# Kernel tuning notes

Measured on AMD Instinct MI355X. Metric: run time of the kernel, lower is better.

Reference implementation:

```python
import jax, jax.numpy as jnp
import numpy as np

B, N, H, D, F = 32, 128, 256, 256, 512   # batch, nodes, gru hidden, latent dim, mlp hidden
SUP = 0.5                                 # ancestor_suppression_strength
EPS = 1e-6


def _gru(x, h, Wx, Wh, bx, bh):
    """torch.nn.GRUCell math; x,h: [..., H]."""
    gx = x @ Wx + bx
    gh = h @ Wh + bh
    rx, ux, nx = jnp.split(gx, 3, axis=-1)
    rh, uh, nh = jnp.split(gh, 3, axis=-1)
    r = jax.nn.sigmoid(rx + rh)
    u = jax.nn.sigmoid(ux + uh)
    n = jnp.tanh(nx + r * nh)
    return (1.0 - u) * n + u * h


def setup_inputs() -> dict:
    key = jax.random.key(0)
    ks = jax.random.split(key, 12)
    rn = lambda k, shape, fan: jax.random.normal(k, shape, jnp.float32) * (fan ** -0.5)
    return {
        "z": jax.random.normal(ks[0], (B, D), jnp.float32),
        "targets": jax.random.randint(ks[1], (B, N, N), 0, 2, jnp.int32),
        "W_init": rn(ks[2], (D, H), D),
        "b_init": jnp.zeros((H,), jnp.float32),
        "Wx": rn(ks[3], (H, 3 * H), H),
        "Wh": rn(ks[4], (H, 3 * H), H),
        "bx": jnp.zeros((3 * H,), jnp.float32),
        "bh": jnp.zeros((3 * H,), jnp.float32),
        "W1": rn(ks[5], (2 * H + D, F), 2 * H + D),
        "b1": jnp.zeros((F,), jnp.float32),
        "W2": rn(ks[6], (F, 1), F),
        "b2": jnp.zeros((1,), jnp.float32),
    }


def reference(z, targets, W_init, b_init, Wx, Wh, bx, bh, W1, b1, W2, b2):
    # teacher-forcing link targets: strictly lower-triangular (parents have smaller index)
    tgt = jnp.tril(targets.astype(jnp.float32), k=-1)  # [B,N,N]
    idx = jnp.arange(N)

    def decode_one(z1, t1):  # z1:[D], t1:[N,N]
        h0 = jnp.tanh(z1 @ W_init + b_init)                      # decoder_init: z -> node-0 state
        states0 = jnp.zeros((N, H), jnp.float32).at[0].set(h0)
        A0 = jnp.zeros((N, N), jnp.float32)                      # ancestor bitset: A[i,j]=1 iff j ancestor of i

        def step(carry, t):
            states, A, ll = carry
            m = (idx < t).astype(jnp.float32)                    # existing-node mask
            pooled = (states * m[:, None]).sum(0) / m.sum()      # mean aggregation
            h_prov = _gru(pooled, h0, Wx, Wh, bx, bh)            # provisional new-node state
            # parent logits: MLP([h_new, h_j, z]) for every existing node j
            feat = jnp.concatenate([jnp.broadcast_to(h_prov, (N, H)), states,
                                    jnp.broadcast_to(z1, (N, D))], axis=-1)   # [N, 2H+D]
            logits = (jax.nn.relu(feat @ W1 + b1) @ W2 + b2)[:, 0]            # [N]
            row = t1[t]                                          # teacher-forced parents of node t
            anc = jnp.minimum(row @ A, 1.0)                      # j already ancestor of a chosen parent
            q = jnp.clip(jax.nn.sigmoid(logits) * (1.0 - SUP * anc), EPS, 1.0 - EPS)
            ll = ll + (m * (row * jnp.log(q) + (1.0 - row) * jnp.log1p(-q))).sum()
            A = A.at[t].set(jnp.minimum(row + row @ A, 1.0))     # ancestors(t) = parents U their ancestors
            states = states.at[t].set(h_prov)
            m2 = (idx <= t).astype(jnp.float32)[:, None]
            pooled2 = (states * m2).sum(0) / m2.sum()
            upd = _gru(jnp.broadcast_to(pooled2, (N, H)), states, Wx, Wh, bx, bh)
            states = m2 * upd + (1.0 - m2) * states              # propagate info among generated nodes
            return (states, A, ll), None

        (states, A, ll), _ = jax.lax.scan(step, (states0, A0, jnp.zeros((), jnp.float32)),
                                          jnp.arange(1, N))
        return t1, ll                                            # link matrix (teacher forced), log-likelihood

    L, ll = jax.vmap(decode_one)(z, tgt)
    return L, ll
```

## Files before the change

### kernel.cpp

```cpp
#include <hip/hip_runtime.h>
#include <hip/hip_bf16.h>
#include <math.h>

#define Bz 32
#define Nn 128
#define Hh 256
#define Dd 256
#define Ff 512
#define Gg 768
#define NT 512

typedef short v8s __attribute__((ext_vector_type(8)));
typedef float f4  __attribute__((ext_vector_type(4)));
#define MFMA(a,b,c) __builtin_amdgcn_mfma_f32_16x16x32_bf16(a,b,c,0,0,0)

#define WS_H0    0
#define WS_GH0   (WS_H0 + Bz*Hh)
#define WS_ZW1   (WS_GH0 + Bz*Gg)
#define WS_GXP   (WS_ZW1 + Bz*Ff)
#define WS_LOGP  (WS_GXP + Bz*8*Gg)
#define WS_BAR   (WS_LOGP + Bz*8*Nn)
#define WS_XS    (WS_BAR + Bz*32)
#define WS_WB    (WS_XS + Bz*16384)

#define SM_SW    0
#define SM_SST   81920
#define SM_NLDS  147456
#define SM_GXF   155648
#define SM_HPF   158720
#define SM_GX2   159232
#define SM_BASE  159616
#define SM_BHS   159872
#define SM_PSN   160256
#define SM_LOGI  160384
#define SM_RBIT  160896
#define SM_ANCW  160928
#define SM_AMASK 160960
#define SMEM_SZ  163008

__device__ __forceinline__ unsigned short f2bf(float x) {
  unsigned u = __float_as_uint(x);
  u = u + 0x7fffu + ((u >> 16) & 1u);
  return (unsigned short)(u >> 16);
}
__device__ __forceinline__ unsigned pack2(float e, float o) {
  return (unsigned)f2bf(e) | ((unsigned)f2bf(o) << 16);
}
__device__ __forceinline__ unsigned pkbf(float x, float y) {
  __hip_bfloat162 h = __float22bfloat162_rn(make_float2(x, y));
  union { __hip_bfloat162 h; unsigned u; } c; c.h = h; return c.u;
}
__device__ __forceinline__ float bf2f(unsigned short s) {
  return __uint_as_float(((unsigned)s) << 16);
}
__device__ __forceinline__ float sigm(float x) { return 1.0f / (1.0f + __expf(-x)); }
__device__ __forceinline__ float tanh_fast(float x) { return 2.0f / (1.0f + __expf(-2.0f*x)) - 1.0f; }
__device__ __forceinline__ v8s u4v(uint4 q) { union { uint4 q; v8s v; } c; c.q = q; return c.v; }

__device__ __forceinline__ void ast32(unsigned* p, unsigned v) {
  __hip_atomic_store(p, v, __ATOMIC_RELAXED, __HIP_MEMORY_SCOPE_AGENT);
}
__device__ __forceinline__ unsigned ald32(const unsigned* p) {
  return __hip_atomic_load(p, __ATOMIC_RELAXED, __HIP_MEMORY_SCOPE_AGENT);
}
__device__ __forceinline__ void ast64(unsigned long long* p, unsigned long long v) {
  __hip_atomic_store(p, v, __ATOMIC_RELAXED, __HIP_MEMORY_SCOPE_AGENT);
}
__device__ __forceinline__ unsigned long long ald64(const unsigned long long* p) {
  return __hip_atomic_load(p, __ATOMIC_RELAXED, __HIP_MEMORY_SCOPE_AGENT);
}

__device__ __forceinline__ void bbar(unsigned* cnt, unsigned& seq)
{
  __builtin_amdgcn_s_waitcnt(0x0F70);
  __syncthreads();
  seq += 8;
  if (threadIdx.x == 0) {
    __hip_atomic_fetch_add(cnt, 1u, __ATOMIC_RELAXED, __HIP_MEMORY_SCOPE_AGENT);
    while (__hip_atomic_load(cnt, __ATOMIC_RELAXED, __HIP_MEMORY_SCOPE_AGENT) < seq)
      __builtin_amdgcn_s_sleep(1);
  }
  __syncthreads();
}

__global__ void __launch_bounds__(256) prep_init(
    const int* __restrict__ tg, const float* __restrict__ Wx,
    const float* __restrict__ Wh, const float* __restrict__ W1,
    float* __restrict__ ws, float* __restrict__ out)
{
  const int stride = gridDim.x * blockDim.x;
  const int t0 = blockIdx.x * blockDim.x + threadIdx.x;

  for (int i = t0; i < Bz*Nn*Nn; i += stride) {
    int col = i & (Nn-1), row = (i >> 7) & (Nn-1);
    out[i] = (col < row) ? (float)tg[i] : 0.0f;
  }
  for (int i = t0; i < Bz; i += stride) out[Bz*Nn*Nn + i] = 0.0f;

  unsigned* BARu = (unsigned*)(ws + WS_BAR);
  for (int i = t0; i < Bz*32; i += stride) BARu[i] = 0u;

  unsigned* Wb = (unsigned*)(ws + WS_WB);
  for (int i = t0; i < 160*2048; i += stride) {
    int jw = i & 3, l = (i >> 2) & 63, ks = (i >> 8) & 7, nt = i >> 11;
    int k = ks*32 + (l >> 4)*8 + 2*jw;
    int n16 = l & 15;
    float lo, hi;
    if (nt < 48)       { int c = nt*16 + n16;        lo = Wh[k*Gg + c];      hi = Wh[(k+1)*Gg + c]; }
    else if (nt < 80)  { int f = (nt-48)*16 + n16;   lo = W1[(Hh+k)*Ff + f]; hi = W1[(Hh+k+1)*Ff + f]; }
    else if (nt < 128) { int c = (nt-80)*16 + n16;   lo = Wx[k*Gg + c];      hi = Wx[(k+1)*Gg + c]; }
    else               { int f = (nt-128)*16 + n16;  lo = W1[k*Ff + f];      hi = W1[(k+1)*Ff + f]; }
    Wb[i] = pack2(lo, hi);
  }
}

__global__ void __launch_bounds__(256) prep_batch(
    const float* __restrict__ z, const float* __restrict__ Wi,
    const float* __restrict__ bi, const float* __restrict__ Wh,
    const float* __restrict__ bh, const float* __restrict__ W1,
    float* __restrict__ ws)
{
  const int b = blockIdx.x, tid = threadIdx.x;
  __shared__ float zs[Dd], h0s[Hh];
  zs[tid] = z[b*Dd + tid];
  __syncthreads();
  float acc = bi[tid];
  for (int d = 0; d < Dd; ++d) acc = fmaf(zs[d], Wi[d*Hh + tid], acc);
  const float h0 = tanhf(acc);
  h0s[tid] = h0;
  ws[WS_H0 + b*Hh + tid] = h0;
  __syncthreads();
  for (int g = tid; g < Gg; g += 256) {
    float a = bh[g];
    for (int h = 0; h < Hh; ++h) a = fmaf(h0s[h], Wh[h*Gg + g], a);
    ws[WS_GH0 + b*Gg + g] = a;
  }
  for (int f = tid; f < Ff; f += 256) {
    float a = 0.0f;
    for (int d = 0; d < Dd; ++d) a = fmaf(zs[d], W1[(2*Hh + d)*Ff + f], a);
    ws[WS_ZW1 + b*Ff + f] = a;
  }
}

__global__ void __launch_bounds__(NT) decoder_main(
    const int* __restrict__ tg,
    const float* __restrict__ bx, const float* __restrict__ bh,
    const float* __restrict__ b1, const float* __restrict__ W2,
    const float* __restrict__ b2,
    float* __restrict__ ws, float* __restrict__ out)
{
  const int blk = blockIdx.x;
  const int b = blk & 31, r = blk >> 5;
  const int tid = threadIdx.x;
  const int lane = tid & 63, wv = tid >> 6;
  const int c16 = lane & 15, quad = lane >> 4;

  extern __shared__ char smem[];
  uint4* SW4 = (uint4*)(smem + SM_SW);
  unsigned short* SST = (unsigned short*)(smem + SM_SST);
  unsigned long long* SST64 = (unsigned long long*)(smem + SM_SST);
  unsigned short* NLDS = (unsigned short*)(smem + SM_NLDS);
  unsigned* NLDSu = (unsigned*)(smem + SM_NLDS);
  unsigned long long* NLDS64 = (unsigned long long*)(smem + SM_NLDS);
  float* GXF  = (float*)(smem + SM_GXF);
  unsigned short* HPF = (unsigned short*)(smem + SM_HPF);
  float* GX2  = (float*)(smem + SM_GX2);
  float* BASE = (float*)(smem + SM_BASE);
  float* BHS  = (float*)(smem + SM_BHS);
  float* PSN  = (float*)(smem + SM_PSN);
  float* LOGI = (float*)(smem + SM_LOGI);
  unsigned* RBIT  = (unsigned*)(smem + SM_RBIT);
  unsigned* ANCW  = (unsigned*)(smem + SM_ANCW);
  unsigned* AMASK = (unsigned*)(smem + SM_AMASK);

  const float* __restrict__ h0g  = ws + WS_H0  + b*Hh;
  const float* __restrict__ gh0g = ws + WS_GH0 + b*Gg;
  const float* __restrict__ zW1g = ws + WS_ZW1 + b*Ff;
  unsigned* GXPown = (unsigned*)(ws + WS_GXP) + b*8*Gg + r*Gg;
  const unsigned long long* GXP64 = (const unsigned long long*)((unsigned*)(ws + WS_GXP) + b*8*Gg);
  unsigned* LOGPg = (unsigned*)(ws + WS_LOGP) + b*8*Nn;
  unsigned long long* LOGP64 = (unsigned long long*)LOGPg;
  unsigned* bar = (unsigned*)(ws + WS_BAR) + b*32;
  unsigned long long* XS64 = (unsigned long long*)(ws + WS_XS) + b*8192;
  const uint4* WB4 = (const uint4*)(ws + WS_WB);

  for (int i = tid; i < 16384; i += NT) ((unsigned*)SST)[i] = 0u;
  for (int i = tid; i < 5120; i += NT) {
    const int lt = i >> 9, q = i & 511;
    int gt;
    if (lt < 6) { const int gate = lt >> 1, tt = lt & 1; gt = gate*16 + 2*r + tt; }
    else        { gt = 48 + 4*r + (lt - 6); }
    SW4[lt*512 + q] = WB4[gt*512 + q];
  }
  for (int i = tid; i < Nn*4; i += NT) AMASK[i] = 0u;
  if (tid < 96) BHS[tid] = bh[(tid >> 5)*256 + 32*r + (tid & 31)];
  float w2r[4];
  #pragma unroll
  for (int ft = 0; ft < 4; ++ft) w2r[ft] = W2[64*r + ft*16 + c16];
  const float b2v = b2[0];
  unsigned bseq = 0;
  __syncthreads();
  if (tid < Hh) {
    const int c = tid;
    SST[(c>>5)*512 + ((c>>3)&3)*128 + (c&7)] = f2bf(h0g[c]);
  }
  if (tid < 32) PSN[tid] = h0g[32*r + tid];
  __syncthreads();
  {
    union { unsigned u[4]; v8s v; } cv;
    const float4 a0 = *(const float4*)(PSN + quad*8);
    const float4 a1 = *(const float4*)(PSN + quad*8 + 4);
    cv.u[0] = pkbf(a0.x, a0.y); cv.u[1] = pkbf(a0.z, a0.w);
    cv.u[2] = pkbf(a1.x, a1.y); cv.u[3] = pkbf(a1.z, a1.w);
    const v8s avp = cv.v;
    #pragma unroll
    for (int k2 = 0; k2 < 6; ++k2) {
      const int nt = wv*6 + k2;
      f4 c = {0.0f,0.0f,0.0f,0.0f};
      c = MFMA(avp, u4v(WB4[(80 + nt)*512 + r*64 + lane]), c);
      if (quad == 0) ast32(GXPown + nt*16 + c16, __float_as_uint(c[0]));
    }
  }
  if (tid < 128) ast64(XS64 + r*128 + tid, SST64[r*128 + tid]);
  bbar(bar, bseq);

  for (int t = 1; t < Nn; ++t) {
    const int par = (t & 1) * 4;
    const float invt  = 1.0f / (float)t;
    const float invt1 = 1.0f / (float)(t + 1);
    const int Mtot = (t + 16) >> 4;
    const int Mlog = (t + 15) >> 4;
    const int mtc = Mtot - 1;

    for (int i = tid; i < Mlog*1024; i += NT) {
      if (((i >> 7) & 7) != r) SST64[i] = ald64(XS64 + i);
    }
    if (tid < 384) {
      float s0 = 0.0f, s1 = 0.0f;
      #pragma unroll
      for (int rr = 0; rr < 8; ++rr) {
        const unsigned long long v = ald64(GXP64 + rr*384 + tid);
        s0 += __uint_as_float((unsigned)v);
        s1 += __uint_as_float((unsigned)(v >> 32));
      }
      GXF[2*tid]   = s0;
      GXF[2*tid+1] = s1;
    } else {
      const int j = tid - 384;
      const int val = (j < t) ? tg[b*Nn*Nn + t*Nn + j] : 0;
      const unsigned long long bal = __ballot(val != 0);
      if (lane == 0) {
        RBIT[par + (wv - 6)*2]     = (unsigned)bal;
        RBIT[par + (wv - 6)*2 + 1] = (unsigned)(bal >> 32);
      }
      LOGI[j] = 0.0f;
      if (j < 32) PSN[j] = 0.0f;
      if (j < 4) ANCW[par + j] = 0u;
    }
    if (t > 1 && r == ((t - 1) & 7)) {
      const int pp = par ^ 4;
      float term = 0.0f;
      if (tid < (t - 1)) {
        float lsum = b2v;
        #pragma unroll
        for (int rr = 0; rr < 8; ++rr)
          lsum += __uint_as_float(ald32(LOGPg + rr*Nn + tid));
        const float anc = (float)((ANCW[pp + (tid >> 5)] >> (tid & 31)) & 1u);
        float q = sigm(lsum) * (1.0f - 0.5f*anc);
        q = fminf(fmaxf(q, 1e-6f), 1.0f - 1e-6f);
        const unsigned rb = (RBIT[pp + (tid >> 5)] >> (tid & 31)) & 1u;
        term = rb ? logf(q) : log1pf(-q);
      }
      if (wv < 2) {
        #pragma unroll
        for (int off = 32; off; off >>= 1) term += __shfl_down(term, off);
        if (lane == 0) atomicAdd(&out[Bz*Nn*Nn + b], term);
      }
    }
    __syncthreads();

    if (tid < 256) {
      const int hc = tid;
      const float rv = sigm(GXF[hc]*invt + bx[hc] + gh0g[hc]);
      const float uv = sigm(GXF[256+hc]*invt + bx[256+hc] + gh0g[256+hc]);
      const float nv = tanh_fast(GXF[512+hc]*invt + bx[512+hc] + rv*gh0g[512+hc]);
      HPF[hc] = f2bf((1.0f - uv)*nv + uv*h0g[hc]);
    } else if (tid < 384) {
      const int j = tid - 256;
      if (j < t && ((RBIT[par + (j >> 5)] >> (j & 31)) & 1u)) {
        atomicOr(&ANCW[par+0], AMASK[j*4+0]); atomicOr(&ANCW[par+1], AMASK[j*4+1]);
        atomicOr(&ANCW[par+2], AMASK[j*4+2]); atomicOr(&ANCW[par+3], AMASK[j*4+3]);
      }
    }
    __syncthreads();

    if (tid < 256) {
      const int c = tid;
      SST[(mtc*8 + (c>>5))*512 + (((c>>3)&3)*16 + (t&15))*8 + (c&7)] = HPF[c];
    } else {
      NLDSu[mtc*256 + (tid - 256)] = 0u;
    }
    if (wv < 2) {
      const unsigned rbv = (RBIT[par + (tid >> 5)] >> (tid & 31)) & 1u;
      const unsigned long long bal = __ballot(tid < t && rbv);
      if (lane == 0) {
        AMASK[t*4 + 2*wv]     = (unsigned)bal         | ANCW[par + 2*wv];
        AMASK[t*4 + 2*wv + 1] = (unsigned)(bal >> 32) | ANCW[par + 2*wv + 1];
      }
    }
    {
      v8s av[8];
      #pragma unroll
      for (int ks = 0; ks < 8; ++ks) av[ks] = *(const v8s*)(HPF + ks*32 + quad*8);
      for (int j = wv; j < 10; j += 8) {
        if (j < 6) {
          const int g = j >> 1, tt = j & 1;
          const uint4* Bp = WB4 + (80 + g*16 + 2*r + tt)*512 + lane;
          f4 c = {0.0f,0.0f,0.0f,0.0f};
          #pragma unroll
          for (int ks = 0; ks < 8; ++ks) c = MFMA(av[ks], u4v(Bp[ks*64]), c);
          if (quad == 0) {
            const int col = g*256 + 32*r + tt*16 + c16;
            GX2[g*32 + tt*16 + c16] = (c[0] + GXF[col])*invt1 + bx[col];
          }
        } else {
          const int ft = j - 6;
          const uint4* Bp = WB4 + (128 + 4*r + ft)*512 + lane;
          f4 c = {0.0f,0.0f,0.0f,0.0f};
          #pragma unroll
          for (int ks = 0; ks < 8; ++ks) c = MFMA(av[ks], u4v(Bp[ks*64]), c);
          if (quad == 0) {
            const int f = 64*r + ft*16 + c16;
            BASE[ft*16 + c16] = c[0] + zW1g[f] + b1[f];
          }
        }
      }
    }
    __syncthreads();

    const int nG = (Mtot + 1) >> 1;
    const int nL = (Mlog + 1) >> 1;
    const int njobs = nG + nL;
    for (int j = wv; j < njobs; j += 8) {
      if (j < nG) {
        const int mt0 = 2*j, mt1 = mt0 + 1;
        const bool do1 = (mt1 < Mtot);
        f4 acc[12];
        #pragma unroll
        for (int i = 0; i < 12; ++i) acc[i] = (f4){0.0f,0.0f,0.0f,0.0f};
        #pragma unroll
        for (int ks = 0; ks < 8; ++ks) {
          const v8s a0 = *(const v8s*)(SST + (mt0*8 + ks)*512 + lane*8);
          const v8s b0 = u4v(SW4[(0*8 + ks)*64 + lane]);
          const v8s b1v = u4v(SW4[(1*8 + ks)*64 + lane]);
          const v8s b2v2 = u4v(SW4[(2*8 + ks)*64 + lane]);
          const v8s b3 = u4v(SW4[(3*8 + ks)*64 + lane]);
          const v8s b4 = u4v(SW4[(4*8 + ks)*64 + lane]);
          const v8s b5 = u4v(SW4[(5*8 + ks)*64 + lane]);
          acc[0] = MFMA(a0, b0, acc[0]); acc[1] = MFMA(a0, b1v, acc[1]);
          acc[2] = MFMA(a0, b2v2, acc[2]); acc[3] = MFMA(a0, b3, acc[3]);
          acc[4] = MFMA(a0, b4, acc[4]); acc[5] = MFMA(a0, b5, acc[5]);
          if (do1) {
            const v8s a1 = *(const v8s*)(SST + (mt1*8 + ks)*512 + lane*8);
            acc[6]  = MFMA(a1, b0, acc[6]);  acc[7]  = MFMA(a1, b1v, acc[7]);
            acc[8]  = MFMA(a1, b2v2, acc[8]);  acc[9]  = MFMA(a1, b3, acc[9]);
            acc[10] = MFMA(a1, b4, acc[10]); acc[11] = MFMA(a1, b5, acc[11]);
          }
        }
        #pragma unroll
        for (int s = 0; s < 2; ++s) {
          if (s == 1 && !do1) break;
          const int mt = s ? mt1 : mt0;
          const f4* ac = acc + 6*s;
          #pragma unroll
          for (int ct = 0; ct < 2; ++ct) {
            const int hcl = ct*16 + c16;
            const f4 cr = ac[0 + ct], cu = ac[2 + ct], cn = ac[4 + ct];
            const float gxr = GX2[hcl], gxu = GX2[32+hcl], gxn = GX2[64+hcl];
            const float bhr = BHS[hcl], bhu = BHS[32+hcl], bhn = BHS[64+hcl];
            float colsum = 0.0f;
            #pragma unroll
            for (int rg = 0; rg < 4; ++rg) {
              const int row = mt*16 + quad*4 + rg;
              if (row <= t) {
                const int spi = ((hcl>>3)*16 + quad*4 + rg)*8 + (hcl & 7);
                const float old = bf2f(SST[(mt*8 + r)*512 + spi]);
                const float rv = sigm(gxr + cr[rg] + bhr);
                const float uv = sigm(gxu + cu[rg] + bhu);
                const float nv = tanh_fast(gxn + rv*(cn[rg] + bhn));
                const float ns = (1.0f-uv)*nv + uv*old;
                NLDS[mt*512 + spi] = f2bf(ns);
                colsum += ns;
              }
            }
            colsum += __shfl_down(colsum, 16);
            colsum += __shfl_down(colsum, 32);
            if (lane < 16) atomicAdd(&PSN[ct*16 + lane], colsum);
          }
        }
      } else {
        const int jj = j - nG;
        const int mt0 = 2*jj, mt1 = mt0 + 1;
        const bool do1 = (mt1 < Mlog);
        f4 acc[8];
        #pragma unroll
        for (int i = 0; i < 8; ++i) acc[i] = (f4){0.0f,0.0f,0.0f,0.0f};
        #pragma unroll
        for (int ks = 0; ks < 8; ++ks) {
          const v8s a0 = *(const v8s*)(SST + (mt0*8 + ks)*512 + lane*8);
          const v8s c0 = u4v(SW4[(6*8 + ks)*64 + lane]);
          const v8s c1 = u4v(SW4[(7*8 + ks)*64 + lane]);
          const v8s c2 = u4v(SW4[(8*8 + ks)*64 + lane]);
          const v8s c3 = u4v(SW4[(9*8 + ks)*64 + lane]);
          acc[0] = MFMA(a0, c0, acc[0]); acc[1] = MFMA(a0, c1, acc[1]);
          acc[2] = MFMA(a0, c2, acc[2]); acc[3] = MFMA(a0, c3, acc[3]);
          if (do1) {
            const v8s a1 = *(const v8s*)(SST + (mt1*8 + ks)*512 + lane*8);
            acc[4] = MFMA(a1, c0, acc[4]); acc[5] = MFMA(a1, c1, acc[5]);
            acc[6] = MFMA(a1, c2, acc[6]); acc[7] = MFMA(a1, c3, acc[7]);
          }
        }
        #pragma unroll
        for (int s = 0; s < 2; ++s) {
          if (s == 1 && !do1) break;
          const int mt = s ? mt1 : mt0;
          const f4* ac = acc + 4*s;
          #pragma unroll
          for (int rg = 0; rg < 4; ++rg) {
            float v = fmaxf(ac[0][rg] + BASE[c16],    0.0f)*w2r[0]
                    + fmaxf(ac[1][rg] + BASE[16+c16], 0.0f)*w2r[1]
                    + fmaxf(ac[2][rg] + BASE[32+c16], 0.0f)*w2r[2]
                    + fmaxf(ac[3][rg] + BASE[48+c16], 0.0f)*w2r[3];
            v += __shfl_xor(v, 1); v += __shfl_xor(v, 2);
            v += __shfl_xor(v, 4); v += __shfl_xor(v, 8);
            const int row = mt*16 + quad*4 + rg;
            if (c16 == 0 && row < t) atomicAdd(&LOGI[row], v);
          }
        }
      }
    }
    __syncthreads();

    {
      union { unsigned u[4]; v8s v; } cv;
      const float4 a0 = *(const float4*)(PSN + quad*8);
      const float4 a1 = *(const float4*)(PSN + quad*8 + 4);
      cv.u[0] = pkbf(a0.x, a0.y); cv.u[1] = pkbf(a0.z, a0.w);
      cv.u[2] = pkbf(a1.x, a1.y); cv.u[3] = pkbf(a1.z, a1.w);
      const v8s avp = cv.v;
      #pragma unroll
      for (int k2 = 0; k2 < 6; ++k2) {
        const int nt = wv*6 + k2;
        f4 c = {0.0f,0.0f,0.0f,0.0f};
        c = MFMA(avp, u4v(WB4[(80 + nt)*512 + r*64 + lane]), c);
        if (quad == 0) ast32(GXPown + nt*16 + c16, __float_as_uint(c[0]));
      }
    }
    for (int i = tid; i < Mtot*128; i += NT) {
      const int mt = i >> 7, q = i & 127;
      const unsigned long long v = NLDS64[i];
      ast64(XS64 + (mt*8 + r)*128 + q, v);
      SST64[(mt*8 + r)*128 + q] = v;
    }
    if (tid < 64) ast64(LOGP64 + r*64 + tid, ((const unsigned long long*)LOGI)[tid]);
    bbar(bar, bseq);
  }

  if (r == 7) {
    const int tl = Nn - 1;
    const int pp = (tl & 1) * 4;
    float term = 0.0f;
    if (tid < tl) {
      float lsum = b2v;
      #pragma unroll
      for (int rr = 0; rr < 8; ++rr)
        lsum += __uint_as_float(ald32(LOGPg + rr*Nn + tid));
      const float anc = (float)((ANCW[pp + (tid >> 5)] >> (tid & 31)) & 1u);
      float q = sigm(lsum) * (1.0f - 0.5f*anc);
      q = fminf(fmaxf(q, 1e-6f), 1.0f - 1e-6f);
      const unsigned rb = (RBIT[pp + (tid >> 5)] >> (tid & 31)) & 1u;
      term = rb ? logf(q) : log1pf(-q);
    }
    if (wv < 2) {
      #pragma unroll
      for (int off = 32; off; off >>= 1) term += __shfl_down(term, off);
      if (lane == 0) atomicAdd(&out[Bz*Nn*Nn + b], term);
    }
  }
}

extern "C" void kernel_launch(void* const* d_in, const int* in_sizes, int n_in,
                              void* d_out, int out_size, void* d_ws, size_t ws_size,
                              hipStream_t stream)
{
  const float* z  = (const float*)d_in[0];
  const int*   tg = (const int*)  d_in[1];
  const float* Wi = (const float*)d_in[2];
  const float* bi = (const float*)d_in[3];
  const float* Wx = (const float*)d_in[4];
  const float* Wh = (const float*)d_in[5];
  const float* bx = (const float*)d_in[6];
  const float* bh = (const float*)d_in[7];
  const float* W1 = (const float*)d_in[8];
  const float* b1 = (const float*)d_in[9];
  const float* W2 = (const float*)d_in[10];
  const float* b2 = (const float*)d_in[11];
  float* out = (float*)d_out;
  float* ws  = (float*)d_ws;

  hipFuncSetAttribute((const void*)decoder_main,
                      hipFuncAttributeMaxDynamicSharedMemorySize, SMEM_SZ);

  hipLaunchKernelGGL(prep_init, dim3(512), dim3(256), 0, stream, tg, Wx, Wh, W1, ws, out);
  hipLaunchKernelGGL(prep_batch, dim3(Bz), dim3(256), 0, stream, z, Wi, bi, Wh, bh, W1, ws);

  void* args[] = { (void*)&tg, (void*)&bx, (void*)&bh, (void*)&b1,
                   (void*)&W2, (void*)&b2, (void*)&ws, (void*)&out };
  hipLaunchCooperativeKernel((void*)decoder_main, dim3(256), dim3(NT),
                             args, SMEM_SZ, stream);
}
```

Before: 2.044 ms.

## Overlap new-node GRU with state-update MFMAs and drop a per-step barrier

Restructures each decode step so waves 0-5 start the existing-node GRU and logit MFMAs immediately after the first barrier. Meanwhile waves 6-7 compute the provisional node state, its own Wh projection (GHT) and the gx/zW1 projections. The new node's GRU update is split out and done separately by one wave. Ancestor-mask propagation moves into the target-loading wave via shuffle-OR, which removes the atomicOr phase and one __syncthreads. The GXP and LOGP exchange buffers are double-buffered by step parity so the log-likelihood reduction can move after the barrier-bracketed section, at the cost of more workspace, more registers and a more intricate job assignment.

```diff
diff --git a/kernel.cpp b/kernel.cpp
--- a/kernel.cpp
+++ b/kernel.cpp
@@ -18,8 +18,8 @@
 #define WS_GH0   (WS_H0 + Bz*Hh)
 #define WS_ZW1   (WS_GH0 + Bz*Gg)
 #define WS_GXP   (WS_ZW1 + Bz*Ff)
-#define WS_LOGP  (WS_GXP + Bz*8*Gg)
-#define WS_BAR   (WS_LOGP + Bz*8*Nn)
+#define WS_LOGP  (WS_GXP + Bz*2*8*Gg)
+#define WS_BAR   (WS_LOGP + Bz*2*8*Nn)
 #define WS_XS    (WS_BAR + Bz*32)
 #define WS_WB    (WS_XS + Bz*16384)
 
@@ -29,14 +29,15 @@
 #define SM_GXF   155648
 #define SM_HPF   158720
 #define SM_GX2   159232
-#define SM_BASE  159616
-#define SM_BHS   159872
-#define SM_PSN   160256
-#define SM_LOGI  160384
-#define SM_RBIT  160896
-#define SM_ANCW  160928
-#define SM_AMASK 160960
-#define SMEM_SZ  163008
+#define SM_GHT   159616
+#define SM_BASE  160000
+#define SM_BHS   160256
+#define SM_PSN   160640
+#define SM_LOGI  160768
+#define SM_RBIT  161280
+#define SM_ANCW  161312
+#define SM_AMASK 161376
+#define SMEM_SZ  163424
 
 __device__ __forceinline__ unsigned short f2bf(float x) {
   unsigned u = __float_as_uint(x);
@@ -142,6 +143,97 @@
   }
 }
 
+__device__ __forceinline__ void G_mfma(const unsigned short* SST, const uint4* SW4,
+    int mt0, bool do1, int lane, f4* acc)
+{
+  #pragma unroll
+  for (int ks = 0; ks < 8; ++ks) {
+    const v8s a0 = *(const v8s*)(SST + (mt0*8 + ks)*512 + lane*8);
+    const v8s w0 = u4v(SW4[(0*8 + ks)*64 + lane]);
+    const v8s w1 = u4v(SW4[(1*8 + ks)*64 + lane]);
+    const v8s w2 = u4v(SW4[(2*8 + ks)*64 + lane]);
+    const v8s w3 = u4v(SW4[(3*8 + ks)*64 + lane]);
+    const v8s w4 = u4v(SW4[(4*8 + ks)*64 + lane]);
+    const v8s w5 = u4v(SW4[(5*8 + ks)*64 + lane]);
+    acc[0] = MFMA(a0,w0,acc[0]); acc[1] = MFMA(a0,w1,acc[1]);
+    acc[2] = MFMA(a0,w2,acc[2]); acc[3] = MFMA(a0,w3,acc[3]);
+    acc[4] = MFMA(a0,w4,acc[4]); acc[5] = MFMA(a0,w5,acc[5]);
+    if (do1) {
+      const v8s a1 = *(const v8s*)(SST + ((mt0+1)*8 + ks)*512 + lane*8);
+      acc[6]  = MFMA(a1,w0,acc[6]);  acc[7]  = MFMA(a1,w1,acc[7]);
+      acc[8]  = MFMA(a1,w2,acc[8]);  acc[9]  = MFMA(a1,w3,acc[9]);
+      acc[10] = MFMA(a1,w4,acc[10]); acc[11] = MFMA(a1,w5,acc[11]);
+    }
+  }
+}
+
+__device__ __forceinline__ void G_epi(const f4* ac, int mt, int t, int r,
+    int quad, int c16, int lane, const float* GX2, const float* BHS,
+    const unsigned short* SST, unsigned short* NLDS, float* PSN)
+{
+  #pragma unroll
+  for (int ct = 0; ct < 2; ++ct) {
+    const int hcl = ct*16 + c16;
+    const f4 cr = ac[0 + ct], cu = ac[2 + ct], cn = ac[4 + ct];
+    const float gxr = GX2[hcl], gxu = GX2[32+hcl], gxn = GX2[64+hcl];
+    const float bhr = BHS[hcl], bhu = BHS[32+hcl], bhn = BHS[64+hcl];
+    float colsum = 0.0f;
+    #pragma unroll
+    for (int rg = 0; rg < 4; ++rg) {
+      const int row = mt*16 + quad*4 + rg;
+      if (row < t) {
+        const int spi = ((hcl>>3)*16 + quad*4 + rg)*8 + (hcl & 7);
+        const float old = bf2f(SST[(mt*8 + r)*512 + spi]);
+        const float rv = sigm(gxr + cr[rg] + bhr);
+        const float uv = sigm(gxu + cu[rg] + bhu);
+        const float nv = tanh_fast(gxn + rv*(cn[rg] + bhn));
+        const float ns = (1.0f-uv)*nv + uv*old;
+        NLDS[mt*512 + spi] = f2bf(ns);
+        colsum += ns;
+      }
+    }
+    colsum += __shfl_down(colsum, 16);
+    colsum += __shfl_down(colsum, 32);
+    if (lane < 16) atomicAdd(&PSN[ct*16 + lane], colsum);
+  }
+}
+
+__device__ __forceinline__ void L_mfma(const unsigned short* SST, const uint4* SW4,
+    int mt0, bool do1, int lane, f4* acc)
+{
+  #pragma unroll
+  for (int ks = 0; ks < 8; ++ks) {
+    const v8s a0 = *(const v8s*)(SST + (mt0*8 + ks)*512 + lane*8);
+    const v8s c0 = u4v(SW4[(6*8 + ks)*64 + lane]);
+    const v8s c1 = u4v(SW4[(7*8 + ks)*64 + lane]);
+    const v8s c2 = u4v(SW4[(8*8 + ks)*64 + lane]);
+    const v8s c3 = u4v(SW4[(9*8 + ks)*64 + lane]);
+    acc[0] = MFMA(a0,c0,acc[0]); acc[1] = MFMA(a0,c1,acc[1]);
+    acc[2] = MFMA(a0,c2,acc[2]); acc[3] = MFMA(a0,c3,acc[3]);
+    if (do1) {
+      const v8s a1 = *(const v8s*)(SST + ((mt0+1)*8 + ks)*512 + lane*8);
+      acc[4] = MFMA(a1,c0,acc[4]); acc[5] = MFMA(a1,c1,acc[5]);
+      acc[6] = MFMA(a1,c2,acc[6]); acc[7] = MFMA(a1,c3,acc[7]);
+    }
+  }
+}
+
+__device__ __forceinline__ void L_epi(const f4* ac, int mt, int t,
+    int quad, int c16, const float* BASE, const float* w2r, float* LOGI)
+{
+  #pragma unroll
+  for (int rg = 0; rg < 4; ++rg) {
+    float v = fmaxf(ac[0][rg] + BASE[c16],    0.0f)*w2r[0]
+            + fmaxf(ac[1][rg] + BASE[16+c16], 0.0f)*w2r[1]
+            + fmaxf(ac[2][rg] + BASE[32+c16], 0.0f)*w2r[2]
+            + fmaxf(ac[3][rg] + BASE[48+c16], 0.0f)*w2r[3];
+    v += __shfl_xor(v, 1); v += __shfl_xor(v, 2);
+    v += __shfl_xor(v, 4); v += __shfl_xor(v, 8);
+    const int row = mt*16 + quad*4 + rg;
+    if (c16 == 0 && row < t) atomicAdd(&LOGI[row], v);
+  }
+}
+
 __global__ void __launch_bounds__(NT) decoder_main(
     const int* __restrict__ tg,
     const float* __restrict__ bx, const float* __restrict__ bh,
@@ -165,6 +257,7 @@
   float* GXF  = (float*)(smem + SM_GXF);
   unsigned short* HPF = (unsigned short*)(smem + SM_HPF);
   float* GX2  = (float*)(smem + SM_GX2);
+  float* GHT  = (float*)(smem + SM_GHT);
   float* BASE = (float*)(smem + SM_BASE);
   float* BHS  = (float*)(smem + SM_BHS);
   float* PSN  = (float*)(smem + SM_PSN);
@@ -176,15 +269,14 @@
   const float* __restrict__ h0g  = ws + WS_H0  + b*Hh;
   const float* __restrict__ gh0g = ws + WS_GH0 + b*Gg;
   const float* __restrict__ zW1g = ws + WS_ZW1 + b*Ff;
-  unsigned* GXPown = (unsigned*)(ws + WS_GXP) + b*8*Gg + r*Gg;
-  const unsigned long long* GXP64 = (const unsigned long long*)((unsigned*)(ws + WS_GXP) + b*8*Gg);
-  unsigned* LOGPg = (unsigned*)(ws + WS_LOGP) + b*8*Nn;
-  unsigned long long* LOGP64 = (unsigned long long*)LOGPg;
+  unsigned* GXPb = (unsigned*)(ws + WS_GXP) + b*2*8*Gg;
+  unsigned* LOGPb = (unsigned*)(ws + WS_LOGP) + b*2*8*Nn;
   unsigned* bar = (unsigned*)(ws + WS_BAR) + b*32;
   unsigned long long* XS64 = (unsigned long long*)(ws + WS_XS) + b*8192;
   const uint4* WB4 = (const uint4*)(ws + WS_WB);
 
   for (int i = tid; i < 16384; i += NT) ((unsigned*)SST)[i] = 0u;
+  for (int i = tid; i < 4096; i += NT) NLDSu[i] = 0u;
   for (int i = tid; i < 5120; i += NT) {
     const int lt = i >> 9, q = i & 511;
     int gt;
@@ -198,6 +290,19 @@
   #pragma unroll
   for (int ft = 0; ft < 4; ++ft) w2r[ft] = W2[64*r + ft*16 + c16];
   const float b2v = b2[0];
+  float p_bx[3][4], p_gh[3][4], p_h0[4];
+  if (wv >= 6) {
+    #pragma unroll
+    for (int k = 0; k < 4; ++k) {
+      const int c = 4*lane + k;
+      p_h0[k] = h0g[c];
+      #pragma unroll
+      for (int g3 = 0; g3 < 3; ++g3) {
+        p_bx[g3][k] = bx[g3*256 + c];
+        p_gh[g3][k] = gh0g[g3*256 + c];
+      }
+    }
+  }
   unsigned bseq = 0;
   __syncthreads();
   if (tid < Hh) {
@@ -213,33 +318,38 @@
     cv.u[0] = pkbf(a0.x, a0.y); cv.u[1] = pkbf(a0.z, a0.w);
     cv.u[2] = pkbf(a1.x, a1.y); cv.u[3] = pkbf(a1.z, a1.w);
     const v8s avp = cv.v;
+    unsigned* GXPw = GXPb + 1*8*Gg + r*Gg;
     #pragma unroll
     for (int k2 = 0; k2 < 6; ++k2) {
       const int nt = wv*6 + k2;
       f4 c = {0.0f,0.0f,0.0f,0.0f};
       c = MFMA(avp, u4v(WB4[(80 + nt)*512 + r*64 + lane]), c);
-      if (quad == 0) ast32(GXPown + nt*16 + c16, __float_as_uint(c[0]));
+      if (quad == 0) ast32(GXPw + nt*16 + c16, __float_as_uint(c[0]));
     }
   }
   if (tid < 128) ast64(XS64 + r*128 + tid, SST64[r*128 + tid]);
   bbar(bar, bseq);
 
   for (int t = 1; t < Nn; ++t) {
-    const int par = (t & 1) * 4;
+    const int tpar = t & 1;
     const float invt  = 1.0f / (float)t;
     const float invt1 = 1.0f / (float)(t + 1);
+    const int Mr   = (t + 15) >> 4;
     const int Mtot = (t + 16) >> 4;
-    const int Mlog = (t + 15) >> 4;
-    const int mtc = Mtot - 1;
-
-    for (int i = tid; i < Mlog*1024; i += NT) {
+    const int mtc  = t >> 4;
+    const int nG = (Mr + 1) >> 1, nL = (Mr + 1) >> 1;
+    const int njobs = nG + nL;
+
+    for (int i = tid; i < Mr*1024; i += NT) {
       if (((i >> 7) & 7) != r) SST64[i] = ald64(XS64 + i);
     }
     if (tid < 384) {
+      const unsigned long long* GXPr =
+          (const unsigned long long*)(GXPb + tpar*8*Gg);
       float s0 = 0.0f, s1 = 0.0f;
       #pragma unroll
       for (int rr = 0; rr < 8; ++rr) {
-        const unsigned long long v = ald64(GXP64 + rr*384 + tid);
+        const unsigned long long v = ald64(GXPr + rr*384 + tid);
         s0 += __uint_as_float((unsigned)v);
         s1 += __uint_as_float((unsigned)(v >> 32));
       }
@@ -250,73 +360,70 @@
       const int val = (j < t) ? tg[b*Nn*Nn + t*Nn + j] : 0;
       const unsigned long long bal = __ballot(val != 0);
       if (lane == 0) {
-        RBIT[par + (wv - 6)*2]     = (unsigned)bal;
-        RBIT[par + (wv - 6)*2 + 1] = (unsigned)(bal >> 32);
+        RBIT[tpar*4 + (wv-6)*2]     = (unsigned)bal;
+        RBIT[tpar*4 + (wv-6)*2 + 1] = (unsigned)(bal >> 32);
       }
       LOGI[j] = 0.0f;
       if (j < 32) PSN[j] = 0.0f;
-      if (j < 4) ANCW[par + j] = 0u;
-    }
-    if (t > 1 && r == ((t - 1) & 7)) {
-      const int pp = par ^ 4;
-      float term = 0.0f;
-      if (tid < (t - 1)) {
-        float lsum = b2v;
-        #pragma unroll
-        for (int rr = 0; rr < 8; ++rr)
-          lsum += __uint_as_float(ald32(LOGPg + rr*Nn + tid));
-        const float anc = (float)((ANCW[pp + (tid >> 5)] >> (tid & 31)) & 1u);
-        float q = sigm(lsum) * (1.0f - 0.5f*anc);
-        q = fminf(fmaxf(q, 1e-6f), 1.0f - 1e-6f);
-        const unsigned rb = (RBIT[pp + (tid >> 5)] >> (tid & 31)) & 1u;
-        term = rb ? logf(q) : log1pf(-q);
-      }
-      if (wv < 2) {
-        #pragma unroll
-        for (int off = 32; off; off >>= 1) term += __shfl_down(term, off);
-        if (lane == 0) atomicAdd(&out[Bz*Nn*Nn + b], term);
+      unsigned m0=0,m1=0,m2=0,m3=0;
+      if (j < t && val != 0) {
+        m0 = AMASK[j*4+0]; m1 = AMASK[j*4+1];
+        m2 = AMASK[j*4+2]; m3 = AMASK[j*4+3];
+      }
+      #pragma unroll
+      for (int off = 1; off < 64; off <<= 1) {
+        m0 |= __shfl_xor(m0, off); m1 |= __shfl_xor(m1, off);
+        m2 |= __shfl_xor(m2, off); m3 |= __shfl_xor(m3, off);
+      }
+      if (lane == 0) {
+        unsigned* aw = ANCW + tpar*8 + (wv-6)*4;
+        aw[0] = m0; aw[1] = m1; aw[2] = m2; aw[3] = m3;
       }
     }
     __syncthreads();
 
-    if (tid < 256) {
-      const int hc = tid;
-      const float rv = sigm(GXF[hc]*invt + bx[hc] + gh0g[hc]);
-      const float uv = sigm(GXF[256+hc]*invt + bx[256+hc] + gh0g[256+hc]);
-      const float nv = tanh_fast(GXF[512+hc]*invt + bx[512+hc] + rv*gh0g[512+hc]);
-      HPF[hc] = f2bf((1.0f - uv)*nv + uv*h0g[hc]);
-    } else if (tid < 384) {
-      const int j = tid - 256;
-      if (j < t && ((RBIT[par + (j >> 5)] >> (j & 31)) & 1u)) {
-        atomicOr(&ANCW[par+0], AMASK[j*4+0]); atomicOr(&ANCW[par+1], AMASK[j*4+1]);
-        atomicOr(&ANCW[par+2], AMASK[j*4+2]); atomicOr(&ANCW[par+3], AMASK[j*4+3]);
-      }
-    }
-    __syncthreads();
-
-    if (tid < 256) {
-      const int c = tid;
-      SST[(mtc*8 + (c>>5))*512 + (((c>>3)&3)*16 + (t&15))*8 + (c&7)] = HPF[c];
+    f4 acc[12];
+    #pragma unroll
+    for (int i = 0; i < 12; ++i) acc[i] = (f4){0.0f,0.0f,0.0f,0.0f};
+    bool haveA = false, d1A = false; int kindA = 0, mtA = 0;
+    if (wv < 6) {
+      if (wv < njobs && wv < 6) {
+        haveA = true;
+        if (wv < nG) { kindA = 0; mtA = 2*wv;       d1A = (mtA + 1 < Mr); }
+        else         { kindA = 1; mtA = 2*(wv-nG);  d1A = (mtA + 1 < Mr); }
+        if (kindA == 0) G_mfma(SST, SW4, mtA, d1A, lane, acc);
+        else            L_mfma(SST, SW4, mtA, d1A, lane, acc);
+      }
     } else {
-      NLDSu[mtc*256 + (tid - 256)] = 0u;
-    }
-    if (wv < 2) {
-      const unsigned rbv = (RBIT[par + (tid >> 5)] >> (tid & 31)) & 1u;
-      const unsigned long long bal = __ballot(tid < t && rbv);
-      if (lane == 0) {
-        AMASK[t*4 + 2*wv]     = (unsigned)bal         | ANCW[par + 2*wv];
-        AMASK[t*4 + 2*wv + 1] = (unsigned)(bal >> 32) | ANCW[par + 2*wv + 1];
-      }
-    }
-    {
+      if (wv == 6 && lane < 4)
+        AMASK[t*4 + lane] = RBIT[tpar*4 + lane] | ANCW[tpar*8 + lane] | ANCW[tpar*8 + 4 + lane];
+      if ((t & 15) == 0) {
+        for (int q = tid - 384; q < 256; q += 128) NLDSu[mtc*256 + q] = 0u;
+      }
+      float hp[4];
+      #pragma unroll
+      for (int k = 0; k < 4; ++k) {
+        const int c = 4*lane + k;
+        const float rv = sigm(GXF[c]*invt       + p_bx[0][k] + p_gh[0][k]);
+        const float uv = sigm(GXF[256+c]*invt   + p_bx[1][k] + p_gh[1][k]);
+        const float nv = tanh_fast(GXF[512+c]*invt + p_bx[2][k] + rv*p_gh[2][k]);
+        hp[k] = (1.0f - uv)*nv + uv*p_h0[k];
+      }
+      uint2 pk;
+      pk.x = pack2(hp[0], hp[1]); pk.y = pack2(hp[2], hp[3]);
+      *(uint2*)((unsigned short*)HPF + 4*lane) = pk;
       v8s av[8];
       #pragma unroll
       for (int ks = 0; ks < 8; ++ks) av[ks] = *(const v8s*)(HPF + ks*32 + quad*8);
-      for (int j = wv; j < 10; j += 8) {
+      for (int j = wv - 6; j < 16; j += 2) {
+        f4 c = {0.0f,0.0f,0.0f,0.0f};
         if (j < 6) {
-          const int g = j >> 1, tt = j & 1;
+          #pragma unroll
+          for (int ks = 0; ks < 8; ++ks) c = MFMA(av[ks], u4v(SW4[(j*8 + ks)*64 + lane]), c);
+          if (quad == 0) GHT[(j>>1)*32 + (j&1)*16 + c16] = c[0];
+        } else if (j < 12) {
+          const int jx = j - 6, g = jx >> 1, tt = jx & 1;
           const uint4* Bp = WB4 + (80 + g*16 + 2*r + tt)*512 + lane;
-          f4 c = {0.0f,0.0f,0.0f,0.0f};
           #pragma unroll
           for (int ks = 0; ks < 8; ++ks) c = MFMA(av[ks], u4v(Bp[ks*64]), c);
           if (quad == 0) {
@@ -324,9 +431,8 @@
             GX2[g*32 + tt*16 + c16] = (c[0] + GXF[col])*invt1 + bx[col];
           }
         } else {
-          const int ft = j - 6;
+          const int ft = j - 12;
           const uint4* Bp = WB4 + (128 + 4*r + ft)*512 + lane;
-          f4 c = {0.0f,0.0f,0.0f,0.0f};
           #pragma unroll
           for (int ks = 0; ks < 8; ++ks) c = MFMA(av[ks], u4v(Bp[ks*64]), c);
           if (quad == 0) {
@@ -338,106 +444,39 @@
     }
     __syncthreads();
 
-    const int nG = (Mtot + 1) >> 1;
-    const int nL = (Mlog + 1) >> 1;
-    const int njobs = nG + nL;
-    for (int j = wv; j < njobs; j += 8) {
-      if (j < nG) {
-        const int mt0 = 2*j, mt1 = mt0 + 1;
-        const bool do1 = (mt1 < Mtot);
-        f4 acc[12];
-        #pragma unroll
-        for (int i = 0; i < 12; ++i) acc[i] = (f4){0.0f,0.0f,0.0f,0.0f};
-        #pragma unroll
-        for (int ks = 0; ks < 8; ++ks) {
-          const v8s a0 = *(const v8s*)(SST + (mt0*8 + ks)*512 + lane*8);
-          const v8s b0 = u4v(SW4[(0*8 + ks)*64 + lane]);
-          const v8s b1v = u4v(SW4[(1*8 + ks)*64 + lane]);
-          const v8s b2v2 = u4v(SW4[(2*8 + ks)*64 + lane]);
-          const v8s b3 = u4v(SW4[(3*8 + ks)*64 + lane]);
-          const v8s b4 = u4v(SW4[(4*8 + ks)*64 + lane]);
-          const v8s b5 = u4v(SW4[(5*8 + ks)*64 + lane]);
-          acc[0] = MFMA(a0, b0, acc[0]); acc[1] = MFMA(a0, b1v, acc[1]);
-          acc[2] = MFMA(a0, b2v2, acc[2]); acc[3] = MFMA(a0, b3, acc[3]);
-          acc[4] = MFMA(a0, b4, acc[4]); acc[5] = MFMA(a0, b5, acc[5]);
-          if (do1) {
-            const v8s a1 = *(const v8s*)(SST + (mt1*8 + ks)*512 + lane*8);
-            acc[6]  = MFMA(a1, b0, acc[6]);  acc[7]  = MFMA(a1, b1v, acc[7]);
-            acc[8]  = MFMA(a1, b2v2, acc[8]);  acc[9]  = MFMA(a1, b3, acc[9]);
-            acc[10] = MFMA(a1, b4, acc[10]); acc[11] = MFMA(a1, b5, acc[11]);
-          }
+    if (wv < 6) {
+      if (haveA) {
+        if (kindA == 0) {
+          G_epi(acc,     mtA,   t, r, quad, c16, lane, GX2, BHS, SST, NLDS, PSN);
+          if (d1A) G_epi(acc+6, mtA+1, t, r, quad, c16, lane, GX2, BHS, SST, NLDS, PSN);
+        } else {
+          L_epi(acc,     mtA,   t, quad, c16, BASE, w2r, LOGI);
+          if (d1A) L_epi(acc+4, mtA+1, t, quad, c16, BASE, w2r, LOGI);
         }
-        #pragma unroll
-        for (int s = 0; s < 2; ++s) {
-          if (s == 1 && !do1) break;
-          const int mt = s ? mt1 : mt0;
-          const f4* ac = acc + 6*s;
+      }
+      if (wv < 2) {
+        const int jB = 6 + wv;
+        if (jB < njobs) {
+          const int mtB = 2*(jB - nG);
+          const bool d1B = (mtB + 1 < Mr);
+          f4 acc2[8];
           #pragma unroll
-          for (int ct = 0; ct < 2; ++ct) {
-            const int hcl = ct*16 + c16;
-            const f4 cr = ac[0 + ct], cu = ac[2 + ct], cn = ac[4 + ct];
-            const float gxr = GX2[hcl], gxu = GX2[32+hcl], gxn = GX2[64+hcl];
-            const float bhr = BHS[hcl], bhu = BHS[32+hcl], bhn = BHS[64+hcl];
-            float colsum = 0.0f;
-            #pragma unroll
-            for (int rg = 0; rg < 4; ++rg) {
-              const int row = mt*16 + quad*4 + rg;
-              if (row <= t) {
-                const int spi = ((hcl>>3)*16 + quad*4 + rg)*8 + (hcl & 7);
-                const float old = bf2f(SST[(mt*8 + r)*512 + spi]);
-                const float rv = sigm(gxr + cr[rg] + bhr);
-                const float uv = sigm(gxu + cu[rg] + bhu);
-                const float nv = tanh_fast(gxn + rv*(cn[rg] + bhn));
-                const float ns = (1.0f-uv)*nv + uv*old;
-                NLDS[mt*512 + spi] = f2bf(ns);
-                colsum += ns;
-              }
-            }
-            colsum += __shfl_down(colsum, 16);
-            colsum += __shfl_down(colsum, 32);
-            if (lane < 16) atomicAdd(&PSN[ct*16 + lane], colsum);
-          }
+          for (int i = 0; i < 8; ++i) acc2[i] = (f4){0.0f,0.0f,0.0f,0.0f};
+          L_mfma(SST, SW4, mtB, d1B, lane, acc2);
+          L_epi(acc2,     mtB,   t, quad, c16, BASE, w2r, LOGI);
+          if (d1B) L_epi(acc2+4, mtB+1, t, quad, c16, BASE, w2r, LOGI);
         }
-      } else {
-        const int jj = j - nG;
-        const int mt0 = 2*jj, mt1 = mt0 + 1;
-        const bool do1 = (mt1 < Mlog);
-        f4 acc[8];
-        #pragma unroll
-        for (int i = 0; i < 8; ++i) acc[i] = (f4){0.0f,0.0f,0.0f,0.0f};
-        #pragma unroll
-        for (int ks = 0; ks < 8; ++ks) {
-          const v8s a0 = *(const v8s*)(SST + (mt0*8 + ks)*512 + lane*8);
-          const v8s c0 = u4v(SW4[(6*8 + ks)*64 + lane]);
-          const v8s c1 = u4v(SW4[(7*8 + ks)*64 + lane]);
-          const v8s c2 = u4v(SW4[(8*8 + ks)*64 + lane]);
-          const v8s c3 = u4v(SW4[(9*8 + ks)*64 + lane]);
-          acc[0] = MFMA(a0, c0, acc[0]); acc[1] = MFMA(a0, c1, acc[1]);
-          acc[2] = MFMA(a0, c2, acc[2]); acc[3] = MFMA(a0, c3, acc[3]);
-          if (do1) {
-            const v8s a1 = *(const v8s*)(SST + (mt1*8 + ks)*512 + lane*8);
-            acc[4] = MFMA(a1, c0, acc[4]); acc[5] = MFMA(a1, c1, acc[5]);
-            acc[6] = MFMA(a1, c2, acc[6]); acc[7] = MFMA(a1, c3, acc[7]);
-          }
-        }
-        #pragma unroll
-        for (int s = 0; s < 2; ++s) {
-          if (s == 1 && !do1) break;
-          const int mt = s ? mt1 : mt0;
-          const f4* ac = acc + 4*s;
-          #pragma unroll
-          for (int rg = 0; rg < 4; ++rg) {
-            float v = fmaxf(ac[0][rg] + BASE[c16],    0.0f)*w2r[0]
-                    + fmaxf(ac[1][rg] + BASE[16+c16], 0.0f)*w2r[1]
-                    + fmaxf(ac[2][rg] + BASE[32+c16], 0.0f)*w2r[2]
-                    + fmaxf(ac[3][rg] + BASE[48+c16], 0.0f)*w2r[3];
-            v += __shfl_xor(v, 1); v += __shfl_xor(v, 2);
-            v += __shfl_xor(v, 4); v += __shfl_xor(v, 8);
-            const int row = mt*16 + quad*4 + rg;
-            if (c16 == 0 && row < t) atomicAdd(&LOGI[row], v);
-          }
-        }
-      }
+      }
+    } else if (wv == 6 && lane < 32) {
+      const int hcl = lane;
+      const float rv = sigm(GX2[hcl]    + GHT[hcl]    + BHS[hcl]);
+      const float uv = sigm(GX2[32+hcl] + GHT[32+hcl] + BHS[32+hcl]);
+      const float nv = tanh_fast(GX2[64+hcl] + rv*(GHT[64+hcl] + BHS[64+hcl]));
+      const float old = bf2f(HPF[32*r + hcl]);
+      const float ns = (1.0f - uv)*nv + uv*old;
+      const int spi = ((hcl>>3)*16 + (t & 15))*8 + (hcl & 7);
+      NLDS[mtc*512 + spi] = f2bf(ns);
+      atomicAdd(&PSN[hcl], ns);
     }
     __syncthreads();
 
@@ -448,12 +487,13 @@
       cv.u[0] = pkbf(a0.x, a0.y); cv.u[1] = pkbf(a0.z, a0.w);
       cv.u[2] = pkbf(a1.x, a1.y); cv.u[3] = pkbf(a1.z, a1.w);
       const v8s avp = cv.v;
+      unsigned* GXPw = GXPb + ((t+1)&1)*8*Gg + r*Gg;
       #pragma unroll
       for (int k2 = 0; k2 < 6; ++k2) {
         const int nt = wv*6 + k2;
         f4 c = {0.0f,0.0f,0.0f,0.0f};
         c = MFMA(avp, u4v(WB4[(80 + nt)*512 + r*64 + lane]), c);
-        if (quad == 0) ast32(GXPown + nt*16 + c16, __float_as_uint(c[0]));
+        if (quad == 0) ast32(GXPw + nt*16 + c16, __float_as_uint(c[0]));
       }
     }
     for (int i = tid; i < Mtot*128; i += NT) {
@@ -462,23 +502,51 @@
       ast64(XS64 + (mt*8 + r)*128 + q, v);
       SST64[(mt*8 + r)*128 + q] = v;
     }
-    if (tid < 64) ast64(LOGP64 + r*64 + tid, ((const unsigned long long*)LOGI)[tid]);
+    if (tid < 64)
+      ast64((unsigned long long*)LOGPb + tpar*512 + r*64 + tid,
+            ((const unsigned long long*)LOGI)[tid]);
+    if (t > 1 && r == ((t - 1) & 7)) {
+      const int pp = (t - 1) & 1;
+      float term = 0.0f;
+      if (tid < (t - 1)) {
+        float lsum = b2v;
+        const unsigned* Lp = LOGPb + pp*1024;
+        #pragma unroll
+        for (int rr = 0; rr < 8; ++rr)
+          lsum += __uint_as_float(ald32(Lp + rr*Nn + tid));
+        const int w = tid >> 5;
+        const unsigned av_ = ANCW[pp*8 + w] | ANCW[pp*8 + 4 + w];
+        const float anc = (float)((av_ >> (tid & 31)) & 1u);
+        float q = sigm(lsum) * (1.0f - 0.5f*anc);
+        q = fminf(fmaxf(q, 1e-6f), 1.0f - 1e-6f);
+        const unsigned rb = (RBIT[pp*4 + w] >> (tid & 31)) & 1u;
+        term = rb ? logf(q) : log1pf(-q);
+      }
+      if (wv < 2) {
+        #pragma unroll
+        for (int off = 32; off; off >>= 1) term += __shfl_down(term, off);
+        if (lane == 0) atomicAdd(&out[Bz*Nn*Nn + b], term);
+      }
+    }
     bbar(bar, bseq);
   }
 
   if (r == 7) {
     const int tl = Nn - 1;
-    const int pp = (tl & 1) * 4;
+    const int pp = tl & 1;
     float term = 0.0f;
     if (tid < tl) {
       float lsum = b2v;
+      const unsigned* Lp = LOGPb + pp*1024;
       #pragma unroll
       for (int rr = 0; rr < 8; ++rr)
-        lsum += __uint_as_float(ald32(LOGPg + rr*Nn + tid));
-      const float anc = (float)((ANCW[pp + (tid >> 5)] >> (tid & 31)) & 1u);
+        lsum += __uint_as_float(ald32(Lp + rr*Nn + tid));
+      const int w = tid >> 5;
+      const unsigned av_ = ANCW[pp*8 + w] | ANCW[pp*8 + 4 + w];
+      const float anc = (float)((av_ >> (tid & 31)) & 1u);
       float q = sigm(lsum) * (1.0f - 0.5f*anc);
       q = fminf(fmaxf(q, 1e-6f), 1.0f - 1e-6f);
-      const unsigned rb = (RBIT[pp + (tid >> 5)] >> (tid & 31)) & 1u;
+      const unsigned rb = (RBIT[pp*4 + w] >> (tid & 31)) & 1u;
       term = rb ? logf(q) : log1pf(-q);
     }
     if (wv < 2) {
```

Result: faster. 1.968 ms (-3.7%).
